# Kernel tuning notes

Hardware: AMD Instinct MI355X
Metric: run time of the kernel (lower is better)

Reference implementation:

```python
import jax, jax.numpy as jnp
import numpy as np

N = 50000   # nodes
E = 800000  # edges (avg degree 16)
H = 4       # heads
IN = 256    # input feature dim
HID = 64    # hidden dim per head (H*HID = 256 = layer-1 indim)
CLS = 40    # num classes


def setup_inputs():
    key = jax.random.key(0)
    ks = jax.random.split(key, 32)
    s = 0.05  # small init scale keeps exp(leaky_relu(...)) numerically tame
    rn = lambda i, shape: jax.random.normal(ks[i], shape, jnp.float32) * s
    inp = {
        'features': jax.random.normal(ks[0], (N, IN), jnp.float32),
        'src': jax.random.randint(ks[1], (E,), 0, N, jnp.int32),
        'dst': jax.random.randint(ks[2], (E,), 0, N, jnp.int32),
        # layer 0 (per-head stacked): fc, attn_l, attn_r
        'W0': rn(3, (H, IN, HID)), 'b0': rn(4, (H, HID)),
        'al0': rn(5, (H, HID)), 'alb0': rn(6, (H,)),
        'ar0': rn(7, (H, HID)), 'arb0': rn(8, (H,)),
        # layer 1 (indim = H*HID = 256), with residual fc per head
        'W1': rn(9, (H, H * HID, HID)), 'b1': rn(10, (H, HID)),
        'al1': rn(11, (H, HID)), 'alb1': rn(12, (H,)),
        'ar1': rn(13, (H, HID)), 'arb1': rn(14, (H,)),
        'R1': rn(15, (H, H * HID, HID)), 'Rb1': rn(16, (H, HID)),
        # final layer (single head, indim = H*HID, outdim = CLS), residual fc
        'Wf': rn(17, (H * HID, CLS)), 'bf': rn(18, (CLS,)),
        'alf': rn(19, (CLS,)), 'alfb': rn(20, (1,)),
        'arf': rn(21, (CLS,)), 'arfb': rn(22, (1,)),
        'Rf': rn(23, (H * HID, CLS)), 'Rbf': rn(24, (CLS,)),
    }
    return inp


def _head(x, W, b, al, alb, ar, arb, src, dst):
    # GATPrepare: ft = Linear(x); a1 = attn_l(ft); a2 = attn_r(ft)
    ft = x @ W + b                              # [N, D]
    a1 = ft @ al + alb                          # [N]
    a2 = ft @ ar + arb                          # [N]
    # edge phase 1: attention = exp(leaky_relu(a2[src] + a1[dst]))
    e = jnp.exp(jax.nn.leaky_relu(a2[src] + a1[dst], 0.01))      # [E]
    # a_sum pass: segment-sum of attention at dst, then normalize (edge softmax)
    denom = jax.ops.segment_sum(e, dst, num_segments=N)          # [N]
    att = (e / denom[dst])[:, None]                              # [E, 1]
    # src_mul_edge + sum: scatter-sum ft[src] * attention into dst
    return jax.ops.segment_sum(ft[src] * att, dst, num_segments=N)  # [N, D]


def reference(features, src, dst,
              W0, b0, al0, alb0, ar0, arb0,
              W1, b1, al1, alb1, ar1, arb1, R1, Rb1,
              Wf, bf, alf, alfb, arf, arfb, Rf, Rbf):
    # layer 0: no residual (hardcoded residual=False for first layer)
    heads = [jax.nn.elu(_head(features, W0[h], b0[h], al0[h], alb0[h], ar0[h], arb0[h], src, dst))
             for h in range(H)]
    x = jnp.concatenate(heads, axis=1)          # [N, H*HID]
    # layer 1: residual via residual_fc (indim != hiddendim)
    heads = [jax.nn.elu(x @ R1[h] + Rb1[h]
                        + _head(x, W1[h], b1[h], al1[h], alb1[h], ar1[h], arb1[h], src, dst))
             for h in range(H)]
    x = jnp.concatenate(heads, axis=1)          # [N, H*HID]
    # final layer: single head to num_classes, residual via residual_fc
    out = jax.nn.elu(x @ Rf + Rbf + _head(x, Wf, bf, alf, alfb, arf, arfb, src, dst))
    return out                                   # [N, CLS]
```

## Files before the change

kernel.cpp:

```cpp
#include <hip/hip_runtime.h>
#include <hip/hip_bf16.h>
#include <math.h>

#define NN   50000
#define NE   800000
#define NHEAD 4
#define HIDD 64
#define DD   256
#define NCLS 40

typedef __attribute__((ext_vector_type(8))) short s8v;
typedef __attribute__((ext_vector_type(4))) float f4v;

static __device__ __forceinline__ float elu_f(float x) {
  return x > 0.f ? x : expm1f(x);
}
static __device__ __forceinline__ float lrelu_exp(float x) {
  float v = x > 0.f ? x : 0.01f * x;
  return expf(v);
}
static __device__ __forceinline__ unsigned short f2bf(float x) {
  union { float f; unsigned u; } v; v.f = x;
  unsigned r = v.u + 0x7fffu + ((v.u >> 16) & 1u);
  return (unsigned short)(r >> 16);
}
static __device__ __forceinline__ float bf2f(unsigned short b) {
  union { unsigned u; float f; } v; v.u = ((unsigned)b) << 16;
  return v.f;
}
static __device__ __forceinline__ float rdlanef(float v, int l) {
  return __uint_as_float(__builtin_amdgcn_readlane(__float_as_uint(v), l));
}

__global__ void pack_all(const float* __restrict__ W0, const float* __restrict__ W1,
                         const float* __restrict__ R1, const float* __restrict__ Wf,
                         const float* __restrict__ Rf,
                         unsigned short* __restrict__ Wp0h, unsigned short* __restrict__ Wp0l,
                         unsigned short* __restrict__ Wp1h, unsigned short* __restrict__ Wp1l,
                         unsigned short* __restrict__ Rp1h, unsigned short* __restrict__ Rp1l,
                         unsigned short* __restrict__ Wfh, unsigned short* __restrict__ Wfl,
                         unsigned short* __restrict__ Rfh, unsigned short* __restrict__ Rfl) {
  int bid = blockIdx.x;
  const float* S; unsigned short *Bh, *Bl; int big;
  if (bid < 256)      { S = W0; Bh = Wp0h; Bl = Wp0l; big = 1; }
  else if (bid < 512) { S = W1; Bh = Wp1h; Bl = Wp1l; big = 1; bid -= 256; }
  else if (bid < 768) { S = R1; Bh = Rp1h; Bl = Rp1l; big = 1; bid -= 512; }
  else if (bid < 832) { S = Wf; Bh = Wfh;  Bl = Wfl;  big = 0; bid -= 768; }
  else                { S = Rf; Bh = Rfh;  Bl = Rfl;  big = 0; bid -= 832; }
  int i = bid * 256 + threadIdx.x;
  int n = i >> 8, k = i & 255;
  float v;
  if (big) v = S[(n >> 6) * (256 * 64) + k * 64 + (n & 63)];
  else     v = (n < NCLS) ? S[k * NCLS + n] : 0.f;
  unsigned short hi = f2bf(v);
  Bh[i] = hi;
  Bl[i] = f2bf(v - bf2f(hi));
}

__global__ void split_bf(const float* __restrict__ A,
                         unsigned short* __restrict__ Ah,
                         unsigned short* __restrict__ Al, int n4) {
  int i = blockIdx.x * 256 + threadIdx.x;
  if (i >= n4) return;
  float4 v = ((const float4*)A)[i];
  ushort4 h, l;
  h.x = f2bf(v.x); l.x = f2bf(v.x - bf2f(h.x));
  h.y = f2bf(v.y); l.y = f2bf(v.y - bf2f(h.y));
  h.z = f2bf(v.z); l.z = f2bf(v.z - bf2f(h.z));
  h.w = f2bf(v.w); l.w = f2bf(v.w - bf2f(h.w));
  ((ushort4*)Ah)[i] = h;
  ((ushort4*)Al)[i] = l;
}

template <int BN, int OBF>
__global__ __launch_bounds__(256) void gemm_bf16x3(
    const unsigned short* __restrict__ Ah, const unsigned short* __restrict__ Al,
    const unsigned short* __restrict__ Bth, const unsigned short* __restrict__ Btl,
    const float* __restrict__ bias, float* __restrict__ C,
    unsigned short* __restrict__ Cb,
    int M, int Nc) {
  constexpr int K = 256;
  constexpr int RS = 40;
  constexpr int WM = (BN == 128) ? 2 : 4;
  constexpr int WN = 4 / WM;
  constexpr int MI = (128 / WM) / 16;
  constexpr int NI = (BN / WN) / 16;

  __shared__ unsigned short sAh[128 * RS];
  __shared__ unsigned short sAl[128 * RS];
  __shared__ unsigned short sBh[BN * RS];
  __shared__ unsigned short sBl[BN * RS];

  const int tid = threadIdx.x;
  const int lane = tid & 63;
  const int w = tid >> 6;
  const int wr = w / WN, wc = w % WN;
  const int rowbase = wr * (128 / WM);
  const int colbase = wc * (BN / WN);
  const int row0 = blockIdx.x * 128;
  const int col0 = blockIdx.y * BN;
  const int lm = lane & 15;
  const int lk8 = (lane >> 4) * 8;

  f4v acc[MI][NI];
#pragma unroll
  for (int i = 0; i < MI; i++)
#pragma unroll
    for (int j = 0; j < NI; j++) acc[i][j] = (f4v)(0.f);

  for (int k0 = 0; k0 < K; k0 += 32) {
    __syncthreads();
#pragma unroll
    for (int i = 0; i < 2; ++i) {
      int idx = tid + i * 256;
      int r = idx >> 2, seg = idx & 3;
      int grow = row0 + r;
      s8v hv = (s8v)(short)0, lv = (s8v)(short)0;
      if (grow < M) {
        size_t g = (size_t)grow * K + k0 + seg * 8;
        hv = *(const s8v*)(Ah + g);
        lv = *(const s8v*)(Al + g);
      }
      *(s8v*)&sAh[r * RS + seg * 8] = hv;
      *(s8v*)&sAl[r * RS + seg * 8] = lv;
    }
#pragma unroll
    for (int i = 0; i < BN / 64; ++i) {
      int idx = tid + i * 256;
      int n = idx >> 2, seg = idx & 3;
      size_t g = (size_t)(col0 + n) * K + k0 + seg * 8;
      *(s8v*)&sBh[n * RS + seg * 8] = *(const s8v*)(Bth + g);
      *(s8v*)&sBl[n * RS + seg * 8] = *(const s8v*)(Btl + g);
    }
    __syncthreads();

    s8v ah[MI], al_[MI], bh[NI], bl_[NI];
#pragma unroll
    for (int mi = 0; mi < MI; ++mi) {
      int base = (rowbase + mi * 16 + lm) * RS + lk8;
      ah[mi] = *(const s8v*)&sAh[base];
      al_[mi] = *(const s8v*)&sAl[base];
    }
#pragma unroll
    for (int ni = 0; ni < NI; ++ni) {
      int base = (colbase + ni * 16 + lm) * RS + lk8;
      bh[ni] = *(const s8v*)&sBh[base];
      bl_[ni] = *(const s8v*)&sBl[base];
    }
#pragma unroll
    for (int mi = 0; mi < MI; ++mi)
#pragma unroll
      for (int ni = 0; ni < NI; ++ni)
        acc[mi][ni] = __builtin_amdgcn_mfma_f32_16x16x32_bf16(ah[mi], bh[ni], acc[mi][ni], 0, 0, 0);
#pragma unroll
    for (int mi = 0; mi < MI; ++mi)
#pragma unroll
      for (int ni = 0; ni < NI; ++ni)
        acc[mi][ni] = __builtin_amdgcn_mfma_f32_16x16x32_bf16(ah[mi], bl_[ni], acc[mi][ni], 0, 0, 0);
#pragma unroll
    for (int mi = 0; mi < MI; ++mi)
#pragma unroll
      for (int ni = 0; ni < NI; ++ni)
        acc[mi][ni] = __builtin_amdgcn_mfma_f32_16x16x32_bf16(al_[mi], bh[ni], acc[mi][ni], 0, 0, 0);
  }

#pragma unroll
  for (int ni = 0; ni < NI; ++ni) {
    int col = col0 + colbase + ni * 16 + lm;
    if (col >= Nc) continue;
    float bv = bias[col];
#pragma unroll
    for (int mi = 0; mi < MI; ++mi) {
      int rbase = row0 + rowbase + mi * 16 + (lane >> 4) * 4;
#pragma unroll
      for (int r = 0; r < 4; ++r) {
        int row = rbase + r;
        if (row < M) {
          float o = acc[mi][ni][r] + bv;
          if (OBF) Cb[(size_t)row * Nc + col] = f2bf(o);
          else     C[(size_t)row * Nc + col] = o;
        }
      }
    }
  }
}

__global__ void attn_scores4_bf(const unsigned short* __restrict__ ftb,
                                const float* __restrict__ al, const float* __restrict__ alb,
                                const float* __restrict__ ar, const float* __restrict__ arb,
                                float* __restrict__ a1, float* __restrict__ a2, int n_nodes) {
  int n = blockIdx.x * 4 + (threadIdx.x >> 6);
  if (n >= n_nodes) return;
  int lane = threadIdx.x & 63;
  ushort4 fb = *(const ushort4*)(ftb + (size_t)n * 256 + lane * 4);
  float4 f = make_float4(bf2f(fb.x), bf2f(fb.y), bf2f(fb.z), bf2f(fb.w));
  float4 l4 = *(const float4*)(al + lane * 4);
  float4 r4 = *(const float4*)(ar + lane * 4);
  float p1 = f.x * l4.x + f.y * l4.y + f.z * l4.z + f.w * l4.w;
  float p2 = f.x * r4.x + f.y * r4.y + f.z * r4.z + f.w * r4.w;
#pragma unroll
  for (int m = 1; m < 16; m <<= 1) {
    p1 += __shfl_xor(p1, m);
    p2 += __shfl_xor(p2, m);
  }
  if ((lane & 15) == 0) {
    int h = lane >> 4;
    a1[n * 4 + h] = p1 + alb[h];
    a2[n * 4 + h] = p2 + arb[h];
  }
}

__global__ void attn_scores1(const float* __restrict__ ftf,
                             const float* __restrict__ alf, const float* __restrict__ alfb,
                             const float* __restrict__ arf, const float* __restrict__ arfb,
                             float* __restrict__ a1, float* __restrict__ a2, int n_nodes) {
  int n = blockIdx.x * 4 + (threadIdx.x >> 6);
  if (n >= n_nodes) return;
  int lane = threadIdx.x & 63;
  float v = (lane < NCLS) ? ftf[(size_t)n * NCLS + lane] : 0.f;
  float p1 = (lane < NCLS) ? v * alf[lane] : 0.f;
  float p2 = (lane < NCLS) ? v * arf[lane] : 0.f;
#pragma unroll
  for (int m = 1; m < 64; m <<= 1) {
    p1 += __shfl_xor(p1, m);
    p2 += __shfl_xor(p2, m);
  }
  if (lane == 0) {
    a1[n] = p1 + alfb[0];
    a2[n] = p2 + arfb[0];
  }
}

__global__ void count_deg(const int* __restrict__ dst, int* __restrict__ deg) {
  int e = blockIdx.x * blockDim.x + threadIdx.x;
  if (e < NE) atomicAdd(&deg[dst[e]], 1);
}

__global__ void scan_deg(const int* __restrict__ deg, int* __restrict__ row_ptr,
                         int* __restrict__ cursor, int n) {
  __shared__ int partials[1024];
  int t = threadIdx.x;
  int chunk = (n + 1023) >> 10;
  int base = t * chunk;
  int lim = min(base + chunk, n);
  int sum = 0;
  for (int i = base; i < lim; ++i) sum += deg[i];
  partials[t] = sum;
  __syncthreads();
  for (int off = 1; off < 1024; off <<= 1) {
    int v = (t >= off) ? partials[t - off] : 0;
    __syncthreads();
    partials[t] += v;
    __syncthreads();
  }
  int run = (t == 0) ? 0 : partials[t - 1];
  if (t == 0) row_ptr[0] = 0;
  for (int i = base; i < lim; ++i) {
    cursor[i] = run;
    run += deg[i];
    row_ptr[i + 1] = run;
  }
}

__global__ void scatter_e(const int* __restrict__ dst, int* __restrict__ cursor,
                          int* __restrict__ eidx) {
  int e = blockIdx.x * blockDim.x + threadIdx.x;
  if (e >= NE) return;
  int d = dst[e];
  int pos = atomicAdd(&cursor[d], 1);
  eidx[pos] = e;
}

__global__ __launch_bounds__(256) void gather_wave4(
    const unsigned short* __restrict__ ftb, const float* __restrict__ a1,
    const float* __restrict__ a2, const float* __restrict__ res,
    const int* __restrict__ row_ptr, const int* __restrict__ eidx,
    const int* __restrict__ src,
    unsigned short* __restrict__ outh, unsigned short* __restrict__ outl) {
  __shared__ float s_w[4][64][4];
  const int wid = threadIdx.x >> 6;
  const int n = blockIdx.x * 4 + wid;
  if (n >= NN) return;
  const int lane = threadIdx.x & 63;
  const int h = lane >> 4;
  const int b = row_ptr[n], en = row_ptr[n + 1];
  const int deg = en - b;
  const float4 a1v = *(const float4*)(a1 + (size_t)n * 4);
  float4 accv = make_float4(0.f, 0.f, 0.f, 0.f);
  float den = 0.f;

  for (int cb = 0; cb < deg; cb += 64) {
    int cnt = min(64, deg - cb);
    int s = 0;
    if (lane < cnt) {
      s = src[eidx[b + cb + lane]];
      float4 as_ = *(const float4*)(a2 + (size_t)s * 4);
      float4 w4;
      w4.x = lrelu_exp(as_.x + a1v.x);
      w4.y = lrelu_exp(as_.y + a1v.y);
      w4.z = lrelu_exp(as_.z + a1v.z);
      w4.w = lrelu_exp(as_.w + a1v.w);
      *(float4*)&s_w[wid][lane][0] = w4;
    }
    asm volatile("s_waitcnt lgkmcnt(0)" ::: "memory");
    int i = 0;
    for (; i + 8 <= cnt; i += 8) {
      int s0 = __builtin_amdgcn_readlane(s, i + 0);
      int s1 = __builtin_amdgcn_readlane(s, i + 1);
      int s2 = __builtin_amdgcn_readlane(s, i + 2);
      int s3 = __builtin_amdgcn_readlane(s, i + 3);
      int s4 = __builtin_amdgcn_readlane(s, i + 4);
      int s5 = __builtin_amdgcn_readlane(s, i + 5);
      int s6 = __builtin_amdgcn_readlane(s, i + 6);
      int s7 = __builtin_amdgcn_readlane(s, i + 7);
      float w0 = s_w[wid][i + 0][h];
      float w1 = s_w[wid][i + 1][h];
      float w2 = s_w[wid][i + 2][h];
      float w3 = s_w[wid][i + 3][h];
      float w4_ = s_w[wid][i + 4][h];
      float w5 = s_w[wid][i + 5][h];
      float w6 = s_w[wid][i + 6][h];
      float w7 = s_w[wid][i + 7][h];
      ushort4 f0 = *(const ushort4*)(ftb + (size_t)s0 * DD + lane * 4);
      ushort4 f1 = *(const ushort4*)(ftb + (size_t)s1 * DD + lane * 4);
      ushort4 f2 = *(const ushort4*)(ftb + (size_t)s2 * DD + lane * 4);
      ushort4 f3 = *(const ushort4*)(ftb + (size_t)s3 * DD + lane * 4);
      ushort4 f4 = *(const ushort4*)(ftb + (size_t)s4 * DD + lane * 4);
      ushort4 f5 = *(const ushort4*)(ftb + (size_t)s5 * DD + lane * 4);
      ushort4 f6 = *(const ushort4*)(ftb + (size_t)s6 * DD + lane * 4);
      ushort4 f7 = *(const ushort4*)(ftb + (size_t)s7 * DD + lane * 4);
      accv.x = fmaf(bf2f(f0.x), w0, accv.x);
      accv.y = fmaf(bf2f(f0.y), w0, accv.y);
      accv.z = fmaf(bf2f(f0.z), w0, accv.z);
      accv.w = fmaf(bf2f(f0.w), w0, accv.w);
      accv.x = fmaf(bf2f(f1.x), w1, accv.x);
      accv.y = fmaf(bf2f(f1.y), w1, accv.y);
      accv.z = fmaf(bf2f(f1.z), w1, accv.z);
      accv.w = fmaf(bf2f(f1.w), w1, accv.w);
      accv.x = fmaf(bf2f(f2.x), w2, accv.x);
      accv.y = fmaf(bf2f(f2.y), w2, accv.y);
      accv.z = fmaf(bf2f(f2.z), w2, accv.z);
      accv.w = fmaf(bf2f(f2.w), w2, accv.w);
      accv.x = fmaf(bf2f(f3.x), w3, accv.x);
      accv.y = fmaf(bf2f(f3.y), w3, accv.y);
      accv.z = fmaf(bf2f(f3.z), w3, accv.z);
      accv.w = fmaf(bf2f(f3.w), w3, accv.w);
      accv.x = fmaf(bf2f(f4.x), w4_, accv.x);
      accv.y = fmaf(bf2f(f4.y), w4_, accv.y);
      accv.z = fmaf(bf2f(f4.z), w4_, accv.z);
      accv.w = fmaf(bf2f(f4.w), w4_, accv.w);
      accv.x = fmaf(bf2f(f5.x), w5, accv.x);
      accv.y = fmaf(bf2f(f5.y), w5, accv.y);
      accv.z = fmaf(bf2f(f5.z), w5, accv.z);
      accv.w = fmaf(bf2f(f5.w), w5, accv.w);
      accv.x = fmaf(bf2f(f6.x), w6, accv.x);
      accv.y = fmaf(bf2f(f6.y), w6, accv.y);
      accv.z = fmaf(bf2f(f6.z), w6, accv.z);
      accv.w = fmaf(bf2f(f6.w), w6, accv.w);
      accv.x = fmaf(bf2f(f7.x), w7, accv.x);
      accv.y = fmaf(bf2f(f7.y), w7, accv.y);
      accv.z = fmaf(bf2f(f7.z), w7, accv.z);
      accv.w = fmaf(bf2f(f7.w), w7, accv.w);
      den += ((w0 + w1) + (w2 + w3)) + ((w4_ + w5) + (w6 + w7));
    }
    for (; i < cnt; ++i) {
      int si = __builtin_amdgcn_readlane(s, i);
      float wi = s_w[wid][i][h];
      ushort4 fv = *(const ushort4*)(ftb + (size_t)si * DD + lane * 4);
      accv.x = fmaf(bf2f(fv.x), wi, accv.x);
      accv.y = fmaf(bf2f(fv.y), wi, accv.y);
      accv.z = fmaf(bf2f(fv.z), wi, accv.z);
      accv.w = fmaf(bf2f(fv.w), wi, accv.w);
      den += wi;
    }
  }
  float invden = (deg > 0) ? 1.f / den : 0.f;
  float4 r = (res != nullptr) ? *(const float4*)(res + (size_t)n * DD + lane * 4)
                              : make_float4(0.f, 0.f, 0.f, 0.f);
  float4 o;
  o.x = elu_f(r.x + accv.x * invden);
  o.y = elu_f(r.y + accv.y * invden);
  o.z = elu_f(r.z + accv.z * invden);
  o.w = elu_f(r.w + accv.w * invden);
  ushort4 hh, ll;
  hh.x = f2bf(o.x); ll.x = f2bf(o.x - bf2f(hh.x));
  hh.y = f2bf(o.y); ll.y = f2bf(o.y - bf2f(hh.y));
  hh.z = f2bf(o.z); ll.z = f2bf(o.z - bf2f(hh.z));
  hh.w = f2bf(o.w); ll.w = f2bf(o.w - bf2f(hh.w));
  *(ushort4*)(outh + (size_t)n * DD + lane * 4) = hh;
  *(ushort4*)(outl + (size_t)n * DD + lane * 4) = ll;
}

__global__ __launch_bounds__(64) void gather_fused1(
    const float* __restrict__ ft, const float* __restrict__ a1,
    const float* __restrict__ a2, const float* __restrict__ res,
    const int* __restrict__ row_ptr, const int* __restrict__ eidx,
    const int* __restrict__ src, float* __restrict__ out) {
  const int n = blockIdx.x;
  const int d = threadIdx.x;
  const int b = row_ptr[n], en = row_ptr[n + 1];
  const int deg = en - b;
  const float a1n = a1[n];
  float acc = 0.f;
  float den = 0.f;

  for (int cb = 0; cb < deg; cb += 64) {
    int cnt = min(64, deg - cb);
    int s = 0;
    float wv = 0.f;
    if (d < cnt) {
      s = src[eidx[b + cb + d]];
      wv = lrelu_exp(a2[s] + a1n);
    }
    int i = 0;
    for (; i + 8 <= cnt; i += 8) {
      int s0 = __builtin_amdgcn_readlane(s, i + 0);
      int s1 = __builtin_amdgcn_readlane(s, i + 1);
      int s2 = __builtin_amdgcn_readlane(s, i + 2);
      int s3 = __builtin_amdgcn_readlane(s, i + 3);
      int s4 = __builtin_amdgcn_readlane(s, i + 4);
      int s5 = __builtin_amdgcn_readlane(s, i + 5);
      int s6 = __builtin_amdgcn_readlane(s, i + 6);
      int s7 = __builtin_amdgcn_readlane(s, i + 7);
      float w0 = rdlanef(wv, i + 0), w1 = rdlanef(wv, i + 1);
      float w2 = rdlanef(wv, i + 2), w3 = rdlanef(wv, i + 3);
      float w4_ = rdlanef(wv, i + 4), w5 = rdlanef(wv, i + 5);
      float w6 = rdlanef(wv, i + 6), w7 = rdlanef(wv, i + 7);
      if (d < NCLS) {
        float v0 = ft[(size_t)s0 * NCLS + d];
        float v1 = ft[(size_t)s1 * NCLS + d];
        float v2 = ft[(size_t)s2 * NCLS + d];
        float v3 = ft[(size_t)s3 * NCLS + d];
        float v4 = ft[(size_t)s4 * NCLS + d];
        float v5 = ft[(size_t)s5 * NCLS + d];
        float v6 = ft[(size_t)s6 * NCLS + d];
        float v7 = ft[(size_t)s7 * NCLS + d];
        acc = fmaf(v0, w0, acc);
        acc = fmaf(v1, w1, acc);
        acc = fmaf(v2, w2, acc);
        acc = fmaf(v3, w3, acc);
        acc = fmaf(v4, w4_, acc);
        acc = fmaf(v5, w5, acc);
        acc = fmaf(v6, w6, acc);
        acc = fmaf(v7, w7, acc);
      }
      den += ((w0 + w1) + (w2 + w3)) + ((w4_ + w5) + (w6 + w7));
    }
    for (; i < cnt; ++i) {
      int si = __builtin_amdgcn_readlane(s, i);
      float wi = rdlanef(wv, i);
      if (d < NCLS) acc = fmaf(ft[(size_t)si * NCLS + d], wi, acc);
      den += wi;
    }
  }
  float invden = (deg > 0) ? 1.f / den : 0.f;
  if (d < NCLS) {
    float r = res[(size_t)n * NCLS + d];
    out[(size_t)n * NCLS + d] = elu_f(r + acc * invden);
  }
}

extern "C" void kernel_launch(void* const* d_in, const int* in_sizes, int n_in,
                              void* d_out, int out_size, void* d_ws, size_t ws_size,
                              hipStream_t stream) {
  const float* features = (const float*)d_in[0];
  const int* src = (const int*)d_in[1];
  const int* dst = (const int*)d_in[2];
  const float* W0 = (const float*)d_in[3];
  const float* b0 = (const float*)d_in[4];
  const float* al0 = (const float*)d_in[5];
  const float* alb0 = (const float*)d_in[6];
  const float* ar0 = (const float*)d_in[7];
  const float* arb0 = (const float*)d_in[8];
  const float* W1 = (const float*)d_in[9];
  const float* b1 = (const float*)d_in[10];
  const float* al1 = (const float*)d_in[11];
  const float* alb1 = (const float*)d_in[12];
  const float* ar1 = (const float*)d_in[13];
  const float* arb1 = (const float*)d_in[14];
  const float* R1 = (const float*)d_in[15];
  const float* Rb1 = (const float*)d_in[16];
  const float* Wf = (const float*)d_in[17];
  const float* bfc = (const float*)d_in[18];
  const float* alf = (const float*)d_in[19];
  const float* alfb = (const float*)d_in[20];
  const float* arf = (const float*)d_in[21];
  const float* arfb = (const float*)d_in[22];
  const float* Rf = (const float*)d_in[23];
  const float* Rbf = (const float*)d_in[24];
  float* out = (float*)d_out;

  float* p = (float*)d_ws;
  float* B1 = p;  p += (size_t)NN * 256;
  float* B2 = p;  p += (size_t)NN * 256;
  float* B3 = p;  p += (size_t)NN * 256;
  float* a1 = p;  p += (size_t)NN * 4;
  float* a2 = p;  p += (size_t)NN * 4;
  unsigned short* us = (unsigned short*)p;
  unsigned short* Wp0h = us; us += 65536;
  unsigned short* Wp0l = us; us += 65536;
  unsigned short* Wp1h = us; us += 65536;
  unsigned short* Wp1l = us; us += 65536;
  unsigned short* Rp1h = us; us += 65536;
  unsigned short* Rp1l = us; us += 65536;
  unsigned short* Wfh = us;  us += 64 * 256;
  unsigned short* Wfl = us;  us += 64 * 256;
  unsigned short* Rfh = us;  us += 64 * 256;
  unsigned short* Rfl = us;  us += 64 * 256;
  unsigned short* Ah = us;   us += (size_t)NN * 256;
  unsigned short* Al = us;   us += (size_t)NN * 256;
  unsigned short* ftb = us;  us += (size_t)NN * 256;
  int* ip = (int*)us;
  int* row_ptr = ip; ip += NN + 1;
  int* cursor = ip;  ip += NN;
  int* deg = ip;     ip += NN;
  int* eidx = ip;    ip += NE;

  const int EB = (NE + 255) / 256;
  const int N4 = NN * 64;

  pack_all<<<896, 256, 0, stream>>>(W0, W1, R1, Wf, Rf,
                                    Wp0h, Wp0l, Wp1h, Wp1l, Rp1h, Rp1l,
                                    Wfh, Wfl, Rfh, Rfl);

  hipMemsetAsync(deg, 0, NN * sizeof(int), stream);
  count_deg<<<EB, 256, 0, stream>>>(dst, deg);
  scan_deg<<<1, 1024, 0, stream>>>(deg, row_ptr, cursor, NN);
  scatter_e<<<EB, 256, 0, stream>>>(dst, cursor, eidx);

  const int MB = (NN + 127) / 128;
  dim3 gbig(MB, 2);
  dim3 gsm(MB, 1);
  const int GW = (NN + 3) / 4;

  split_bf<<<(N4 + 255) / 256, 256, 0, stream>>>(features, Ah, Al, N4);
  gemm_bf16x3<128, 1><<<gbig, 256, 0, stream>>>(Ah, Al, Wp0h, Wp0l, b0, nullptr, ftb, NN, 256);
  attn_scores4_bf<<<(NN + 3) / 4, 256, 0, stream>>>(ftb, al0, alb0, ar0, arb0, a1, a2, NN);
  gather_wave4<<<GW, 256, 0, stream>>>(ftb, a1, a2, nullptr, row_ptr, eidx, src, Ah, Al);

  gemm_bf16x3<128, 1><<<gbig, 256, 0, stream>>>(Ah, Al, Wp1h, Wp1l, b1, nullptr, ftb, NN, 256);
  gemm_bf16x3<128, 0><<<gbig, 256, 0, stream>>>(Ah, Al, Rp1h, Rp1l, Rb1, B3, nullptr, NN, 256);
  attn_scores4_bf<<<(NN + 3) / 4, 256, 0, stream>>>(ftb, al1, alb1, ar1, arb1, a1, a2, NN);
  gather_wave4<<<GW, 256, 0, stream>>>(ftb, a1, a2, B3, row_ptr, eidx, src, Ah, Al);

  gemm_bf16x3<64, 0><<<gsm, 256, 0, stream>>>(Ah, Al, Wfh, Wfl, bfc, B1, nullptr, NN, NCLS);
  gemm_bf16x3<64, 0><<<gsm, 256, 0, stream>>>(Ah, Al, Rfh, Rfl, Rbf, B2, nullptr, NN, NCLS);
  attn_scores1<<<(NN + 3) / 4, 256, 0, stream>>>(B1, alf, alfb, arf, arfb, a1, a2, NN);
  gather_fused1<<<NN, 64, 0, stream>>>(B1, a1, a2, B2, row_ptr, eidx, src, out);
}
```

Measured before the change: 746.5 us.

## Fuse final-layer GEMMs into one launch and parallelize degree scan

Packs the final-layer Wf and Rf weights into one 128-column matrix so a single BN=128 GEMM computes both the attention features and the residual projection, reading the bf16 hi/lo activations once instead of twice. It also replaces the single-block 1024-thread degree scan with a three-kernel multi-block scan (block partial sums, a serial top-level scan, then a block-local scan and write). The intent is to cut redundant activation reads and the serial bottleneck of the one-block scan. In exchange it adds two extra small launches and a column-split epilogue.

After: 641.3 us. 14.1% less time.

```diff
diff --git a/kernel.cpp b/kernel.cpp
--- a/kernel.cpp
+++ b/kernel.cpp
@@ -38,20 +38,23 @@
                          unsigned short* __restrict__ Wp0h, unsigned short* __restrict__ Wp0l,
                          unsigned short* __restrict__ Wp1h, unsigned short* __restrict__ Wp1l,
                          unsigned short* __restrict__ Rp1h, unsigned short* __restrict__ Rp1l,
-                         unsigned short* __restrict__ Wfh, unsigned short* __restrict__ Wfl,
-                         unsigned short* __restrict__ Rfh, unsigned short* __restrict__ Rfl) {
+                         unsigned short* __restrict__ WfRh, unsigned short* __restrict__ WfRl) {
   int bid = blockIdx.x;
-  const float* S; unsigned short *Bh, *Bl; int big;
+  const float* S = nullptr; unsigned short *Bh, *Bl; int big;
   if (bid < 256)      { S = W0; Bh = Wp0h; Bl = Wp0l; big = 1; }
   else if (bid < 512) { S = W1; Bh = Wp1h; Bl = Wp1l; big = 1; bid -= 256; }
   else if (bid < 768) { S = R1; Bh = Rp1h; Bl = Rp1l; big = 1; bid -= 512; }
-  else if (bid < 832) { S = Wf; Bh = Wfh;  Bl = Wfl;  big = 0; bid -= 768; }
-  else                { S = Rf; Bh = Rfh;  Bl = Rfl;  big = 0; bid -= 832; }
+  else                { Bh = WfRh; Bl = WfRl; big = 0; bid -= 768; }
   int i = bid * 256 + threadIdx.x;
   int n = i >> 8, k = i & 255;
   float v;
-  if (big) v = S[(n >> 6) * (256 * 64) + k * 64 + (n & 63)];
-  else     v = (n < NCLS) ? S[k * NCLS + n] : 0.f;
+  if (big) {
+    v = S[(n >> 6) * (256 * 64) + k * 64 + (n & 63)];
+  } else {
+    int cc = n & 63;
+    const float* SS = (n < 64) ? Wf : Rf;
+    v = (cc < NCLS) ? SS[k * NCLS + cc] : 0.f;
+  }
   unsigned short hi = f2bf(v);
   Bh[i] = hi;
   Bl[i] = f2bf(v - bf2f(hi));
@@ -72,11 +75,12 @@
   ((ushort4*)Al)[i] = l;
 }
 
-template <int BN, int OBF>
+template <int BN, int MODE>
 __global__ __launch_bounds__(256) void gemm_bf16x3(
     const unsigned short* __restrict__ Ah, const unsigned short* __restrict__ Al,
     const unsigned short* __restrict__ Bth, const unsigned short* __restrict__ Btl,
-    const float* __restrict__ bias, float* __restrict__ C,
+    const float* __restrict__ bias, const float* __restrict__ bias2,
+    float* __restrict__ C, float* __restrict__ C2,
     unsigned short* __restrict__ Cb,
     int M, int Nc) {
   constexpr int K = 256;
@@ -167,18 +171,34 @@
 #pragma unroll
   for (int ni = 0; ni < NI; ++ni) {
     int col = col0 + colbase + ni * 16 + lm;
-    if (col >= Nc) continue;
-    float bv = bias[col];
-#pragma unroll
-    for (int mi = 0; mi < MI; ++mi) {
-      int rbase = row0 + rowbase + mi * 16 + (lane >> 4) * 4;
-#pragma unroll
-      for (int r = 0; r < 4; ++r) {
-        int row = rbase + r;
-        if (row < M) {
-          float o = acc[mi][ni][r] + bv;
-          if (OBF) Cb[(size_t)row * Nc + col] = f2bf(o);
-          else     C[(size_t)row * Nc + col] = o;
+    if (MODE != 2) {
+      if (col >= Nc) continue;
+      float bv = bias[col];
+#pragma unroll
+      for (int mi = 0; mi < MI; ++mi) {
+        int rbase = row0 + rowbase + mi * 16 + (lane >> 4) * 4;
+#pragma unroll
+        for (int r = 0; r < 4; ++r) {
+          int row = rbase + r;
+          if (row < M) {
+            float o = acc[mi][ni][r] + bv;
+            if (MODE == 1) Cb[(size_t)row * Nc + col] = f2bf(o);
+            else           C[(size_t)row * Nc + col] = o;
+          }
+        }
+      }
+    } else {
+      int cc = col & 63;
+      if (cc >= NCLS) continue;
+      float bv = (col < 64) ? bias[cc] : bias2[cc];
+      float* dstp = (col < 64) ? C : C2;
+#pragma unroll
+      for (int mi = 0; mi < MI; ++mi) {
+        int rbase = row0 + rowbase + mi * 16 + (lane >> 4) * 4;
+#pragma unroll
+        for (int r = 0; r < 4; ++r) {
+          int row = rbase + r;
+          if (row < M) dstp[(size_t)row * NCLS + cc] = acc[mi][ni][r] + bv;
         }
       }
     }
@@ -236,30 +256,57 @@
   if (e < NE) atomicAdd(&deg[dst[e]], 1);
 }
 
-__global__ void scan_deg(const int* __restrict__ deg, int* __restrict__ row_ptr,
-                         int* __restrict__ cursor, int n) {
-  __shared__ int partials[1024];
+__global__ void scan_part(const int* __restrict__ deg, int* __restrict__ bsum, int n) {
+  __shared__ int red[256];
   int t = threadIdx.x;
-  int chunk = (n + 1023) >> 10;
-  int base = t * chunk;
-  int lim = min(base + chunk, n);
-  int sum = 0;
-  for (int i = base; i < lim; ++i) sum += deg[i];
-  partials[t] = sum;
+  int base = blockIdx.x * 1024 + t * 4;
+  int s = 0;
+#pragma unroll
+  for (int j = 0; j < 4; ++j) {
+    int idx = base + j;
+    if (idx < n) s += deg[idx];
+  }
+  red[t] = s;
   __syncthreads();
-  for (int off = 1; off < 1024; off <<= 1) {
-    int v = (t >= off) ? partials[t - off] : 0;
+  for (int off = 128; off > 0; off >>= 1) {
+    if (t < off) red[t] += red[t + off];
     __syncthreads();
-    partials[t] += v;
+  }
+  if (t == 0) bsum[blockIdx.x] = red[0];
+}
+
+__global__ void scan_top(const int* __restrict__ bsum, int* __restrict__ boff, int nb) {
+  if (threadIdx.x == 0) {
+    int run = 0;
+    for (int i = 0; i < nb; ++i) { boff[i] = run; run += bsum[i]; }
+  }
+}
+
+__global__ void scan_write(const int* __restrict__ deg, const int* __restrict__ boff,
+                           int* __restrict__ row_ptr, int* __restrict__ cursor, int n) {
+  __shared__ int tsum[256];
+  int t = threadIdx.x;
+  int base = blockIdx.x * 1024 + t * 4;
+  int d0 = 0, d1 = 0, d2 = 0, d3 = 0;
+  if (base + 0 < n) d0 = deg[base + 0];
+  if (base + 1 < n) d1 = deg[base + 1];
+  if (base + 2 < n) d2 = deg[base + 2];
+  if (base + 3 < n) d3 = deg[base + 3];
+  int s = d0 + d1 + d2 + d3;
+  tsum[t] = s;
+  __syncthreads();
+  for (int off = 1; off < 256; off <<= 1) {
+    int u = (t >= off) ? tsum[t - off] : 0;
     __syncthreads();
-  }
-  int run = (t == 0) ? 0 : partials[t - 1];
-  if (t == 0) row_ptr[0] = 0;
-  for (int i = base; i < lim; ++i) {
-    cursor[i] = run;
-    run += deg[i];
-    row_ptr[i + 1] = run;
-  }
+    tsum[t] += u;
+    __syncthreads();
+  }
+  int excl = boff[blockIdx.x] + tsum[t] - s;
+  if (base + 0 < n) { cursor[base + 0] = excl; excl += d0; row_ptr[base + 1] = excl; }
+  if (base + 1 < n) { cursor[base + 1] = excl; excl += d1; row_ptr[base + 2] = excl; }
+  if (base + 2 < n) { cursor[base + 2] = excl; excl += d2; row_ptr[base + 3] = excl; }
+  if (base + 3 < n) { cursor[base + 3] = excl; excl += d3; row_ptr[base + 4] = excl; }
+  if (blockIdx.x == 0 && t == 0) row_ptr[0] = 0;
 }
 
 __global__ void scatter_e(const int* __restrict__ dst, int* __restrict__ cursor,
@@ -503,10 +550,8 @@
   unsigned short* Wp1l = us; us += 65536;
   unsigned short* Rp1h = us; us += 65536;
   unsigned short* Rp1l = us; us += 65536;
-  unsigned short* Wfh = us;  us += 64 * 256;
-  unsigned short* Wfl = us;  us += 64 * 256;
-  unsigned short* Rfh = us;  us += 64 * 256;
-  unsigned short* Rfl = us;  us += 64 * 256;
+  unsigned short* WfRh = us; us += 128 * 256;
+  unsigned short* WfRl = us; us += 128 * 256;
   unsigned short* Ah = us;   us += (size_t)NN * 256;
   unsigned short* Al = us;   us += (size_t)NN * 256;
   unsigned short* ftb = us;  us += (size_t)NN * 256;
@@ -515,17 +560,22 @@
   int* cursor = ip;  ip += NN;
   int* deg = ip;     ip += NN;
   int* eidx = ip;    ip += NE;
+  int* bsum = ip;    ip += 64;
+  int* boff = ip;    ip += 64;
 
   const int EB = (NE + 255) / 256;
   const int N4 = NN * 64;
+  const int GB = (NN + 1023) / 1024;
 
   pack_all<<<896, 256, 0, stream>>>(W0, W1, R1, Wf, Rf,
                                     Wp0h, Wp0l, Wp1h, Wp1l, Rp1h, Rp1l,
-                                    Wfh, Wfl, Rfh, Rfl);
+                                    WfRh, WfRl);
 
   hipMemsetAsync(deg, 0, NN * sizeof(int), stream);
   count_deg<<<EB, 256, 0, stream>>>(dst, deg);
-  scan_deg<<<1, 1024, 0, stream>>>(deg, row_ptr, cursor, NN);
+  scan_part<<<GB, 256, 0, stream>>>(deg, bsum, NN);
+  scan_top<<<1, 64, 0, stream>>>(bsum, boff, GB);
+  scan_write<<<GB, 256, 0, stream>>>(deg, boff, row_ptr, cursor, NN);
   scatter_e<<<EB, 256, 0, stream>>>(dst, cursor, eidx);
 
   const int MB = (NN + 127) / 128;
@@ -534,17 +584,20 @@
   const int GW = (NN + 3) / 4;
 
   split_bf<<<(N4 + 255) / 256, 256, 0, stream>>>(features, Ah, Al, N4);
-  gemm_bf16x3<128, 1><<<gbig, 256, 0, stream>>>(Ah, Al, Wp0h, Wp0l, b0, nullptr, ftb, NN, 256);
+  gemm_bf16x3<128, 1><<<gbig, 256, 0, stream>>>(Ah, Al, Wp0h, Wp0l, b0, nullptr,
+                                                nullptr, nullptr, ftb, NN, 256);
   attn_scores4_bf<<<(NN + 3) / 4, 256, 0, stream>>>(ftb, al0, alb0, ar0, arb0, a1, a2, NN);
   gather_wave4<<<GW, 256, 0, stream>>>(ftb, a1, a2, nullptr, row_ptr, eidx, src, Ah, Al);
 
-  gemm_bf16x3<128, 1><<<gbig, 256, 0, stream>>>(Ah, Al, Wp1h, Wp1l, b1, nullptr, ftb, NN, 256);
-  gemm_bf16x3<128, 0><<<gbig, 256, 0, stream>>>(Ah, Al, Rp1h, Rp1l, Rb1, B3, nullptr, NN, 256);
+  gemm_bf16x3<128, 1><<<gbig, 256, 0, stream>>>(Ah, Al, Wp1h, Wp1l, b1, nullptr,
+                                                nullptr, nullptr, ftb, NN, 256);
+  gemm_bf16x3<128, 0><<<gbig, 256, 0, stream>>>(Ah, Al, Rp1h, Rp1l, Rb1, nullptr,
+                                                B3, nullptr, nullptr, NN, 256);
   attn_scores4_bf<<<(NN + 3) / 4, 256, 0, stream>>>(ftb, al1, alb1, ar1, arb1, a1, a2, NN);
   gather_wave4<<<GW, 256, 0, stream>>>(ftb, a1, a2, B3, row_ptr, eidx, src, Ah, Al);
 
-  gemm_bf16x3<64, 0><<<gsm, 256, 0, stream>>>(Ah, Al, Wfh, Wfl, bfc, B1, nullptr, NN, NCLS);
-  gemm_bf16x3<64, 0><<<gsm, 256, 0, stream>>>(Ah, Al, Rfh, Rfl, Rbf, B2, nullptr, NN, NCLS);
+  gemm_bf16x3<128, 2><<<gsm, 256, 0, stream>>>(Ah, Al, WfRh, WfRl, bfc, Rbf,
+                                               B1, B2, nullptr, NN, 128);
   attn_scores1<<<(NN + 3) / 4, 256, 0, stream>>>(B1, alf, alfb, arf, arfb, a1, a2, NN);
   gather_fused1<<<NN, 64, 0, stream>>>(B1, a1, a2, B2, row_ptr, eidx, src, out);
 }
```
